# Performance work log

Hardware: AMD Instinct MI355X
Metric: run time of the kernel (lower is better)

Reference implementation:

```python
import jax, jax.numpy as jnp
import numpy as np
from jax import lax

B, T, U, L, V = 256, 256, 512, 256, 64


def lstm_layer(x_seq, Wx, Wh, b):
    """Keras LSTMCell math, gate order i,f,g,o. x_seq: [B,T,D] -> [B,T,U], (h,c)."""
    batch = x_seq.shape[0]
    units = Wh.shape[0]
    h0 = jnp.zeros((batch, units), x_seq.dtype)
    c0 = jnp.zeros((batch, units), x_seq.dtype)

    def step(carry, xt):
        h, c = carry
        z = xt @ Wx + h @ Wh + b  # [B,4U]
        i, f, g, o = jnp.split(z, 4, axis=-1)
        i = jax.nn.sigmoid(i)
        f = jax.nn.sigmoid(f)
        g = jnp.tanh(g)
        o = jax.nn.sigmoid(o)
        c = f * c + i * g
        h = o * jnp.tanh(c)
        return (h, c), h

    xs = jnp.swapaxes(x_seq, 0, 1)  # [T,B,D]
    (h, c), ys = lax.scan(step, (h0, c0), xs)
    return jnp.swapaxes(ys, 0, 1), (h, c)


def run_stack(x, Wx0, Wh0, b0, Wx12, Wh12, b12):
    y, (h, c) = lstm_layer(x, Wx0, Wh0, b0)
    for l in range(2):
        y, (h, c) = lstm_layer(y, Wx12[l], Wh12[l], b12[l])
    return y, h


def setup_inputs() -> dict:
    key = jax.random.key(0)
    ks = jax.random.split(key, 24)

    def u(k, shape, s=0.1):
        return jax.random.uniform(k, shape, jnp.float32, -s, s)

    inp = {}
    inp["tokens"] = jax.random.randint(ks[0], (B, T), 0, V, dtype=jnp.int32)
    inp["eps"] = jax.random.normal(ks[1], (B, L), dtype=jnp.float32)
    inp["emb"] = u(ks[2], (L, V))  # embedding table [latent, vocab] as in source
    # encoder LSTM stack (layer0 input dim V; layers 1,2 input dim U)
    inp["enc_Wx0"] = u(ks[3], (V, 4 * U))
    inp["enc_Wh0"] = u(ks[4], (U, 4 * U))
    inp["enc_b0"] = jnp.zeros((4 * U,), jnp.float32)
    inp["enc_Wx12"] = u(ks[5], (2, U, 4 * U))
    inp["enc_Wh12"] = u(ks[6], (2, U, 4 * U))
    inp["enc_b12"] = jnp.zeros((2, 4 * U), jnp.float32)
    # encoder latent heads
    inp["w_mean"] = u(ks[7], (U, L))
    inp["b_mean"] = jnp.zeros((L,), jnp.float32)
    inp["w_sigma"] = u(ks[8], (U, L))
    inp["b_sigma"] = jnp.zeros((L,), jnp.float32)
    # decoder LSTM stack (layer0 input dim L+V)
    inp["dec_Wx0"] = u(ks[9], (L + V, 4 * U))
    inp["dec_Wh0"] = u(ks[10], (U, 4 * U))
    inp["dec_b0"] = jnp.zeros((4 * U,), jnp.float32)
    inp["dec_Wx12"] = u(ks[11], (2, U, 4 * U))
    inp["dec_Wh12"] = u(ks[12], (2, U, 4 * U))
    inp["dec_b12"] = jnp.zeros((2, 4 * U), jnp.float32)
    # decoder output projection
    inp["dec_W"] = u(ks[13], (U, V))
    inp["dec_b"] = jnp.zeros((V,), jnp.float32)
    return inp


def reference(tokens, eps, emb, enc_Wx0, enc_Wh0, enc_b0, enc_Wx12, enc_Wh12,
              enc_b12, w_mean, b_mean, w_sigma, b_sigma, dec_Wx0, dec_Wh0,
              dec_b0, dec_Wx12, dec_Wh12, dec_b12, dec_W, dec_b):
    # embedding lookup: table [L, V] indexed by token ids -> x: [B, T, V]
    x = emb[tokens]
    # encoder: 3-layer LSTM, take final h of last layer
    _, h = run_stack(x, enc_Wx0, enc_Wh0, enc_b0, enc_Wx12, enc_Wh12, enc_b12)
    mean = h @ w_mean + b_mean
    sigma = h @ w_sigma + b_sigma
    latent = mean + jnp.exp(sigma / 2.0) * eps  # reparameterization
    # tile latent over time and concat with embedded inputs
    z = jnp.broadcast_to(latent[:, None, :], (B, T, L))
    dec_in = jnp.concatenate([z, x], axis=-1)  # [B, T, L+V]
    y, _ = run_stack(dec_in, dec_Wx0, dec_Wh0, dec_b0, dec_Wx12, dec_Wh12, dec_b12)
    logits = y @ dec_W + dec_b  # [B, T, V]
    pred = jnp.argmax(logits, axis=2)  # argmax(softmax) == argmax(logits)
    return (pred, logits)
```

## Files before the change

kernel.cpp:

```cpp
#include <hip/hip_runtime.h>
#include <math.h>

#define B 256
#define T 256
#define U 512
#define L 256
#define V 64
#define G4U 2048
#define BU (B * U)
#define HBUF 262144

typedef __attribute__((ext_vector_type(8))) short bf16x8;
typedef __attribute__((ext_vector_type(16))) float f32x16;

__device__ __forceinline__ unsigned short bf16_hi(float x) {
    union { float f; unsigned int u; } c; c.f = x;
    unsigned int r = c.u + 0x7fffu + ((c.u >> 16) & 1u);
    return (unsigned short)(r >> 16);
}
__device__ __forceinline__ float bf16_f(unsigned short h) {
    union { unsigned int u; float f; } c; c.u = ((unsigned int)h) << 16;
    return c.f;
}

__device__ __forceinline__ void st_coh32(void* p, unsigned int v) {
    asm volatile("global_store_dword %0, %1, off sc0 sc1"
                 :: "v"(p), "v"(v) : "memory");
}
__device__ __forceinline__ unsigned int ld_coh32_wait(const void* p) {
    unsigned int r;
    asm volatile("global_load_dword %0, %1, off sc0 sc1\n\t"
                 "s_waitcnt vmcnt(0)"
                 : "=v"(r) : "v"(p) : "memory");
    return r;
}

__device__ __forceinline__ void flags_wait(int* bar, int wmask, int target, int lane)
{
    if (threadIdx.x < 64) {
        #pragma unroll
        for (int r = 0; r < 4; ++r) {
            if (wmask & (1 << r)) {
                const int fi = (r * 64 + lane) * 16;
                while ((int)ld_coh32_wait(&bar[fi]) < target)
                    __builtin_amdgcn_s_sleep(1);
            }
        }
        __builtin_amdgcn_fence(__ATOMIC_ACQUIRE, "agent");
    }
    __syncthreads();
}
__device__ __forceinline__ void flags_pub(int* bar, int bid, int val)
{
    asm volatile("s_waitcnt vmcnt(0)" ::: "memory");
    __syncthreads();
    if (threadIdx.x == 0)
        st_coh32(&bar[bid * 16], (unsigned int)val);
}

__device__ __forceinline__ void gemm4(const unsigned short* __restrict__ abase,
                                      const unsigned short* bhiB,
                                      const unsigned short* bloB,
                                      int kh8, f32x16& acc)
{
    bf16x8 ah[4], al[4];
    #pragma unroll
    for (int i = 0; i < 4; ++i) {
        ah[i] = *(const bf16x8*)(abase + i * 32 + kh8);
        al[i] = *(const bf16x8*)(abase + i * 32 + 16 + kh8);
    }
    #pragma unroll
    for (int i = 0; i < 4; ++i) {
        bf16x8 bh = *(const bf16x8*)(bhiB + i * 512);
        bf16x8 bl = *(const bf16x8*)(bloB + i * 512);
        acc = __builtin_amdgcn_mfma_f32_32x32x16_bf16(ah[i], bh, acc, 0, 0, 0);
        acc = __builtin_amdgcn_mfma_f32_32x32x16_bf16(ah[i], bl, acc, 0, 0, 0);
        acc = __builtin_amdgcn_mfma_f32_32x32x16_bf16(al[i], bh, acc, 0, 0, 0);
    }
}

template<int NCH>
__device__ __forceinline__ void gemm_sub(const unsigned short* __restrict__ abase,
                                         const unsigned short* bhiB,
                                         const unsigned short* bloB,
                                         f32x16& acc)
{
    constexpr int NB = NCH / 8;
    bf16x8 ah[2][8], al[2][8];
    #pragma unroll
    for (int i = 0; i < 8; ++i) {
        ah[0][i] = *(const bf16x8*)(abase + i * 1024);
        al[0][i] = *(const bf16x8*)(abase + i * 1024 + 512);
    }
    #pragma unroll
    for (int b = 0; b < NB; ++b) {
        const int cur = b & 1, nxt = cur ^ 1;
        if (b + 1 < NB) {
            #pragma unroll
            for (int i = 0; i < 8; ++i) {
                const int c = (b + 1) * 8 + i;
                ah[nxt][i] = *(const bf16x8*)(abase + c * 1024);
                al[nxt][i] = *(const bf16x8*)(abase + c * 1024 + 512);
            }
        }
        #pragma unroll
        for (int i = 0; i < 8; ++i) {
            const int c = b * 8 + i;
            bf16x8 bh = *(const bf16x8*)(bhiB + c * 512);
            bf16x8 bl = *(const bf16x8*)(bloB + c * 512);
            acc = __builtin_amdgcn_mfma_f32_32x32x16_bf16(ah[cur][i], bh, acc, 0, 0, 0);
            acc = __builtin_amdgcn_mfma_f32_32x32x16_bf16(ah[cur][i], bl, acc, 0, 0, 0);
            acc = __builtin_amdgcn_mfma_f32_32x32x16_bf16(al[cur][i], bh, acc, 0, 0, 0);
        }
    }
}

__global__ void __launch_bounds__(512, 1)
vae_stack(const unsigned short* __restrict__ xI,
          const float* __restrict__ Wx0, const float* __restrict__ Wh0,
          const float* __restrict__ Wx1, const float* __restrict__ Wh1,
          const float* __restrict__ Wx2, const float* __restrict__ Wh2,
          const float* __restrict__ cb_base, const float* __restrict__ rb0,
          unsigned short* __restrict__ h,
          const float* __restrict__ projW, const float* __restrict__ projB,
          float* __restrict__ out, int nphase, int* __restrict__ bar)
{
    __shared__ __align__(16) char smem[131072];
    const int nb = gridDim.x;
    const int tid = threadIdx.x;
    const int bid = blockIdx.x;
    const int role = bid >> 6;
    const int ug = bid & 63;
    const int lane = tid & 63;
    const int wv = tid >> 6;
    const int m0 = wv * 32;

    const int allmask = (nb == 256) ? 0b1111 : 0b0111;
    int wmask;
    if      (role == 0) wmask = 0b0011;
    else if (role == 1) wmask = 0b0111;
    else if (role == 2) wmask = (nb == 256) ? 0b1110 : 0b0110;
    else                wmask = 0b0100;

    {
        unsigned int* hz = (unsigned int*)h;
        const int stride = nb * 512;
        for (int i = bid * 512 + tid; i < 786432; i += stride)
            st_coh32(hz + i, 0u);
    }

    auto HP = [&](int layer, int buf) -> unsigned short* {
        return h + (size_t)(layer * 2 + buf) * HBUF;
    };

    if (role < 3) {
        const int K  = (role == 0) ? 576 : 1024;
        const int Dx = (role == 0) ? 64 : 512;
        unsigned short* Whi = (unsigned short*)smem;
        unsigned short* Wlo = (unsigned short*)(smem + 65536);

        const float* WxL = (role == 0) ? Wx0 : ((role == 1) ? Wx1 : Wx2);
        const float* WhL = (role == 0) ? Wh0 : ((role == 1) ? Wh1 : Wh2);
        for (int idx = tid; idx < K * 32; idx += 512) {
            int k = idx >> 5, n = idx & 31, u = n >> 2, g = n & 3;
            int col = g * 512 + ug * 8 + u;
            float w = (k < Dx) ? WxL[(size_t)k * G4U + col]
                               : WhL[(size_t)(k - Dx) * G4U + col];
            unsigned short hi = bf16_hi(w);
            int off = ((k >> 3) * 32 + n) * 8 + (k & 7);
            Whi[off] = hi;
            Wlo[off] = bf16_hi(w - bf16_f(hi));
        }

        const bool userb = (role == 0) && (rb0 != nullptr);
        const float colbias = userb ? 0.0f
                            : cb_base[role * 2048 + ug * 32 + (lane & 31)];
        float cst[16];
        #pragma unroll
        for (int i = 0; i < 16; ++i) cst[i] = 0.0f;

        const int arow = m0 + (lane & 31);
        const int kh8  = (lane >> 5) * 8;
        const int frg  = (lane >> 5) * 256 + (lane & 31) * 8;
        const int lf   = (lane & 31) * 16 + (lane >> 5) * 8;
        const size_t mt = (size_t)wv * 32768;

        flags_pub(bar, bid, 1);
        flags_wait(bar, allmask, 1, lane);

        for (int p = 0; p < nphase; ++p) {
            flags_wait(bar, wmask, p + 1, lane);
            const int t = p - role;
            if (t >= 0 && t < T) {
                const int wr = t & 1, rd = wr ^ 1;
                f32x16 acc;
                #pragma unroll
                for (int i = 0; i < 16; ++i) acc[i] = 0.0f;

                if (role == 0) {
                    gemm4(xI + ((size_t)arow * T + t) * 128,
                          Whi + frg, Wlo + frg, kh8, acc);
                    gemm_sub<32>(HP(0, rd) + mt + lf,
                                 Whi + 4 * 512 + frg, Wlo + 4 * 512 + frg, acc);
                } else {
                    gemm_sub<32>(HP(role - 1, wr) + mt + lf,
                                 Whi + frg, Wlo + frg, acc);
                    gemm_sub<32>(HP(role, rd) + mt + lf,
                                 Whi + 32 * 512 + frg, Wlo + 32 * 512 + frg, acc);
                }

                const int n = lane & 31, g = n & 3, u8 = n >> 2, hi5 = lane >> 5;
                unsigned short* hw = HP(role, wr);
                const int gu = ug * 8 + u8;
                const int cg = gu >> 4, eg = gu & 15;
                const bool g1 = (g & 1), g2 = (g & 2);
                const bool store_t = (g == 0) && !(u8 & 1);
                #pragma unroll
                for (int r = 0; r < 16; ++r) {
                    int ri = (r & 3) + 8 * (r >> 2) + 4 * hi5;
                    float z = acc[r] + colbias;
                    if (userb) z += rb0[(size_t)(m0 + ri) * G4U + ug * 32 + n];
                    float zb = __shfl_xor(z, 1, 64);
                    float zc = __shfl_xor(z, 2, 64);
                    float zd = __shfl_xor(z, 3, 64);
                    float t01 = g1 ? zb : z,  t23 = g1 ? zd : zc;
                    float u01 = g1 ? z  : zb, u23 = g1 ? zc : zd;
                    float zi = g2 ? t23 : t01;
                    float zf = g2 ? u23 : u01;
                    float zG = g2 ? t01 : t23;
                    float zo = g2 ? u01 : u23;
                    float ig = 1.0f / (1.0f + expf(-zi));
                    float fg = 1.0f / (1.0f + expf(-zf));
                    float gg = tanhf(zG);
                    float og = 1.0f / (1.0f + expf(-zo));
                    cst[r] = fg * cst[r] + ig * gg;
                    float hv = og * tanhf(cst[r]);
                    unsigned short hh2 = bf16_hi(hv);
                    unsigned short hl2 = bf16_hi(hv - bf16_f(hh2));
                    unsigned int hh_p = (unsigned int)__shfl_xor((int)hh2, 4, 64);
                    unsigned int hl_p = (unsigned int)__shfl_xor((int)hl2, 4, 64);
                    if (store_t) {
                        size_t ho = mt + (size_t)cg * 1024 + ri * 16 + eg;
                        st_coh32(hw + ho,       (unsigned int)hh2 | (hh_p << 16));
                        st_coh32(hw + ho + 512, (unsigned int)hl2 | (hl_p << 16));
                    }
                }
            }
            flags_pub(bar, bid, p + 2);
        }
    } else {
        float* hrow  = (float*)smem;
        float* parts = (float*)(smem + 8192);
        const int b0p = ug * 4;
        const float pbv = projW ? projB[lane] : 0.0f;
        const int r = wv & 3, kp = wv >> 2, v = lane;
        flags_pub(bar, bid, 1);
        flags_wait(bar, allmask, 1, lane);
        for (int p = 0; p < nphase; ++p) {
            flags_wait(bar, wmask, p + 1, lane);
            const int tp = p - 3;
            if (projW && tp >= 0 && tp < T) {
                {
                    int rr = tid >> 7, kq = (tid & 127) * 4;
                    int grow = b0p + rr;
                    int c = kq >> 4, e = kq & 15;
                    const unsigned short* hb2 = HP(2, tp & 1)
                        + (size_t)(grow >> 5) * 32768 + (size_t)c * 1024
                        + (grow & 31) * 16 + e;
                    ushort4 vh = *(const ushort4*)hb2;
                    ushort4 vl = *(const ushort4*)(hb2 + 512);
                    float4 f;
                    f.x = bf16_f(vh.x) + bf16_f(vl.x);
                    f.y = bf16_f(vh.y) + bf16_f(vl.y);
                    f.z = bf16_f(vh.z) + bf16_f(vl.z);
                    f.w = bf16_f(vh.w) + bf16_f(vl.w);
                    *(float4*)(hrow + rr * 512 + kq) = f;
                }
                __syncthreads();
                float acc = 0.0f;
                const float* wp = projW + (size_t)v * 512 + kp * 256;
                const float* hp = hrow + r * 512 + kp * 256;
                #pragma unroll 8
                for (int q = 0; q < 64; ++q) {
                    float4 w  = *(const float4*)(wp + q * 4);
                    float4 hq = *(const float4*)(hp + q * 4);
                    acc = fmaf(w.x, hq.x, acc); acc = fmaf(w.y, hq.y, acc);
                    acc = fmaf(w.z, hq.z, acc); acc = fmaf(w.w, hq.w, acc);
                }
                if (kp == 1) parts[r * 64 + v] = acc;
                __syncthreads();
                if (kp == 0) {
                    float logit = acc + parts[r * 64 + v] + pbv;
                    int grow = b0p + r;
                    __builtin_nontemporal_store(
                        logit, &out[(size_t)B * T + ((size_t)grow * T + tp) * V + v]);
                    float best = logit; int bi = v;
                    #pragma unroll
                    for (int off = 32; off; off >>= 1) {
                        float ov = __shfl_xor(best, off, 64);
                        int oi  = __shfl_xor(bi, off, 64);
                        if (ov > best || (ov == best && oi < bi)) { best = ov; bi = oi; }
                    }
                    if (v == 0)
                        __builtin_nontemporal_store((float)bi,
                                                    &out[(size_t)grow * T + tp]);
                }
            }
            flags_pub(bar, bid, p + 2);
        }
    }
}

__global__ void embed_split_k(const int* __restrict__ tok, const float* __restrict__ emb,
                              unsigned short* __restrict__ xI)
{
    int idx = blockIdx.x * 256 + threadIdx.x;
    int pos = idx >> 4, q = idx & 15;
    int c = q >> 2, kk4 = (q & 3) * 4;
    int tk = tok[pos];
    float4 v = *(const float4*)(emb + (size_t)tk * V + q * 4);
    ushort4 hh, ll;
    hh.x = bf16_hi(v.x); ll.x = bf16_hi(v.x - bf16_f(hh.x));
    hh.y = bf16_hi(v.y); ll.y = bf16_hi(v.y - bf16_f(hh.y));
    hh.z = bf16_hi(v.z); ll.z = bf16_hi(v.z - bf16_f(hh.z));
    hh.w = bf16_hi(v.w); ll.w = bf16_hi(v.w - bf16_f(hh.w));
    size_t base = (size_t)pos * 128 + c * 32 + kk4;
    *(ushort4*)(xI + base) = hh;
    *(ushort4*)(xI + base + 16) = ll;
}

__global__ void latent_k(const unsigned short* __restrict__ h2,
                         const float* __restrict__ eps,
                         const float* __restrict__ wm, const float* __restrict__ bm,
                         const float* __restrict__ wsig, const float* __restrict__ bs,
                         float* __restrict__ lat)
{
    __shared__ float hr[U];
    int b = blockIdx.x, l = threadIdx.x;
    {
        size_t o1 = (size_t)(b >> 5) * 32768 + (size_t)(l >> 4) * 1024
                  + (b & 31) * 16 + (l & 15);
        int l2 = l + 256;
        size_t o2 = (size_t)(b >> 5) * 32768 + (size_t)(l2 >> 4) * 1024
                  + (b & 31) * 16 + (l2 & 15);
        hr[l]  = bf16_f(h2[o1]) + bf16_f(h2[o1 + 512]);
        hr[l2] = bf16_f(h2[o2]) + bf16_f(h2[o2 + 512]);
    }
    __syncthreads();
    float am = bm[l], as = bs[l];
    for (int k = 0; k < U; ++k) {
        float h = hr[k];
        am = fmaf(h, wm[(size_t)k * L + l], am);
        as = fmaf(h, wsig[(size_t)k * L + l], as);
    }
    lat[(size_t)b * L + l] = am + expf(as * 0.5f) * eps[(size_t)b * L + l];
}

__global__ void xcr_k(const float* __restrict__ lat, const float* __restrict__ Wx0,
                      const float* __restrict__ b0v, float* __restrict__ xcr)
{
    __shared__ float lr[L];
    int b = blockIdx.x >> 3;
    int oc = (blockIdx.x & 7) * 256 + threadIdx.x;
    lr[threadIdx.x] = lat[(size_t)b * L + threadIdx.x];
    __syncthreads();
    float acc = b0v[oc];
    for (int k = 0; k < L; ++k) acc = fmaf(lr[k], Wx0[(size_t)k * G4U + oc], acc);
    int g = oc >> 9, rest = oc & 511, ugi = rest >> 3, u = rest & 7;
    xcr[(size_t)b * G4U + ugi * 32 + u * 4 + g] = acc;
}

__global__ void biasref_k(const float* s0, const float* s1, const float* s2,
                          const float* s3, const float* s4, float* __restrict__ ebr)
{
    int idx = blockIdx.x * 256 + threadIdx.x;
    int which = idx >> 11, oc = idx & 2047;
    const float* s = which == 0 ? s0 : which == 1 ? s1 : which == 2 ? s2
                   : which == 3 ? s3 : s4;
    int g = oc >> 9, rest = oc & 511, ugi = rest >> 3, u = rest & 7;
    ebr[which * 2048 + ugi * 32 + u * 4 + g] = s[oc];
}

__global__ void wtprep_k(const float* __restrict__ W, float* __restrict__ Wt)
{
    int idx = blockIdx.x * 256 + threadIdx.x;
    int k = idx >> 6, v = idx & 63;
    Wt[(size_t)v * 512 + k] = W[idx];
}

__global__ void barinit_k(int* __restrict__ bar)
{
    bar[blockIdx.x * 256 + threadIdx.x] = 0;
}

__global__ void sentinel_k(float* __restrict__ out, float val) { out[threadIdx.x] = val; }

extern "C" void kernel_launch(void* const* d_in, const int* in_sizes, int n_in,
                              void* d_out, int out_size, void* d_ws, size_t ws_size,
                              hipStream_t stream)
{
    const int*   tokens   = (const int*)  d_in[0];
    const float* eps      = (const float*)d_in[1];
    const float* emb      = (const float*)d_in[2];
    const float* enc_Wx0  = (const float*)d_in[3];
    const float* enc_Wh0  = (const float*)d_in[4];
    const float* enc_b0   = (const float*)d_in[5];
    const float* enc_Wx12 = (const float*)d_in[6];
    const float* enc_Wh12 = (const float*)d_in[7];
    const float* enc_b12  = (const float*)d_in[8];
    const float* w_mean   = (const float*)d_in[9];
    const float* b_mean   = (const float*)d_in[10];
    const float* w_sigma  = (const float*)d_in[11];
    const float* b_sigma  = (const float*)d_in[12];
    const float* dec_Wx0  = (const float*)d_in[13];
    const float* dec_Wh0  = (const float*)d_in[14];
    const float* dec_b0   = (const float*)d_in[15];
    const float* dec_Wx12 = (const float*)d_in[16];
    const float* dec_Wh12 = (const float*)d_in[17];
    const float* dec_b12  = (const float*)d_in[18];
    const float* dec_W    = (const float*)d_in[19];
    const float* dec_b    = (const float*)d_in[20];
    float* out = (float*)d_out;

    unsigned short* xI  = (unsigned short*)d_ws;
    unsigned short* h   = xI + (size_t)B * T * 128;
    float* lat = (float*)(h + 6 * (size_t)HBUF);
    float* xcr = lat + (size_t)B * L;
    float* ebr = xcr + (size_t)B * G4U;
    float* Wt  = ebr + 5 * G4U;
    int*   bar = (int*)(Wt + 64 * 512);
    size_t need = (size_t)((char*)(bar + 4096) - (char*)d_ws);
    if (ws_size < need) {
        sentinel_k<<<dim3(1), dim3(64), 0, stream>>>(out, -1.0e6f);
        return;
    }

    const size_t UG = (size_t)U * G4U;

    embed_split_k<<<dim3(B * T * 16 / 256), dim3(256), 0, stream>>>(tokens, emb, xI);
    biasref_k<<<dim3(40), dim3(256), 0, stream>>>(enc_b0, enc_b12, enc_b12 + G4U,
                                                  dec_b12, dec_b12 + G4U, ebr);
    wtprep_k<<<dim3(128), dim3(256), 0, stream>>>(dec_W, Wt);

    auto coop = [&](int grid, const float* Wx0_, const float* Wh0_,
                    const float* Wx1_, const float* Wh1_,
                    const float* Wx2_, const float* Wh2_,
                    const float* cbb, const float* rb,
                    const float* pW, const float* pB, int np) -> hipError_t {
        const unsigned short* a_xI = xI;
        unsigned short* a_h = h;
        float* a_out = out;
        int* a_bar = bar;
        void* args[] = { (void*)&a_xI,
                         (void*)&Wx0_, (void*)&Wh0_, (void*)&Wx1_, (void*)&Wh1_,
                         (void*)&Wx2_, (void*)&Wh2_,
                         (void*)&cbb, (void*)&rb, (void*)&a_h,
                         (void*)&pW, (void*)&pB, (void*)&a_out, (void*)&np,
                         (void*)&a_bar };
        return hipLaunchCooperativeKernel((void*)vae_stack, dim3(grid), dim3(512),
                                          args, 0, stream);
    };

    barinit_k<<<dim3(16), dim3(256), 0, stream>>>(bar);
    hipError_t e1 = coop(192, enc_Wx0, enc_Wh0, enc_Wx12, enc_Wh12,
                         enc_Wx12 + UG, enc_Wh12 + UG,
                         ebr, nullptr, nullptr, nullptr, T + 2);

    latent_k<<<dim3(B), dim3(256), 0, stream>>>(h + 5 * (size_t)HBUF,
                                                eps, w_mean, b_mean, w_sigma, b_sigma, lat);
    xcr_k<<<dim3(2048), dim3(256), 0, stream>>>(lat, dec_Wx0, dec_b0, xcr);

    barinit_k<<<dim3(16), dim3(256), 0, stream>>>(bar);
    hipError_t e2 = coop(256, dec_Wx0 + (size_t)L * G4U, dec_Wh0, dec_Wx12, dec_Wh12,
                         dec_Wx12 + UG, dec_Wh12 + UG,
                         ebr + 2 * G4U, xcr, Wt, dec_b, T + 3);

    if (e1 != hipSuccess || e2 != hipSuccess) {
        sentinel_k<<<dim3(1), dim3(64), 0, stream>>>(out, -3.0e6f);
    }
}
```

Baseline: 14.04 ms.

## Use 64-slot hidden-state ring buffers to relax inter-layer wavefront sync

Replaces the double-buffered per-layer hidden state with a 64-slot ring per layer. Each role now waits only on its upstream producer every phase and on its downstream consumer only once it is 56 phases ahead, so layers are no longer held in tight lockstep. The per-phase agent acquire fence is dropped in favour of one fence every 32 phases, relying on coherent sc0/sc1 loads and stores. This costs much more workspace and a larger hidden-state footprint in cache, and the sparser fence risks stale reads if coherence is not guaranteed.

```diff
diff --git a/kernel.cpp b/kernel.cpp
--- a/kernel.cpp
+++ b/kernel.cpp
@@ -7,8 +7,8 @@
 #define L 256
 #define V 64
 #define G4U 2048
-#define BU (B * U)
 #define HBUF 262144
+#define SLOTS 64
 
 typedef __attribute__((ext_vector_type(8))) short bf16x8;
 typedef __attribute__((ext_vector_type(16))) float f32x16;
@@ -46,7 +46,6 @@
                     __builtin_amdgcn_s_sleep(1);
             }
         }
-        __builtin_amdgcn_fence(__ATOMIC_ACQUIRE, "agent");
     }
     __syncthreads();
 }
@@ -56,6 +55,15 @@
     __syncthreads();
     if (threadIdx.x == 0)
         st_coh32(&bar[bid * 16], (unsigned int)val);
+}
+
+__device__ __forceinline__ void ring_fence(int p)
+{
+    if ((p & 31) == 0) {
+        if (threadIdx.x == 0)
+            __builtin_amdgcn_fence(__ATOMIC_ACQUIRE, "agent");
+        __syncthreads();
+    }
 }
 
 __device__ __forceinline__ void gemm4(const unsigned short* __restrict__ abase,
@@ -127,6 +135,7 @@
 {
     __shared__ __align__(16) char smem[131072];
     const int nb = gridDim.x;
+    const bool hasProj = (nb == 256);
     const int tid = threadIdx.x;
     const int bid = blockIdx.x;
     const int role = bid >> 6;
@@ -134,23 +143,19 @@
     const int lane = tid & 63;
     const int wv = tid >> 6;
     const int m0 = wv * 32;
-
-    const int allmask = (nb == 256) ? 0b1111 : 0b0111;
-    int wmask;
-    if      (role == 0) wmask = 0b0011;
-    else if (role == 1) wmask = 0b0111;
-    else if (role == 2) wmask = (nb == 256) ? 0b1110 : 0b0110;
-    else                wmask = 0b0100;
+    const int allmask = hasProj ? 0b1111 : 0b0111;
 
     {
         unsigned int* hz = (unsigned int*)h;
         const int stride = nb * 512;
-        for (int i = bid * 512 + tid; i < 786432; i += stride)
-            st_coh32(hz + i, 0u);
-    }
-
-    auto HP = [&](int layer, int buf) -> unsigned short* {
-        return h + (size_t)(layer * 2 + buf) * HBUF;
+        for (int i = bid * 512 + tid; i < 393216; i += stride) {
+            int l = i >> 17, off = i & 131071;
+            st_coh32(hz + ((size_t)(l * SLOTS + 63) * 131072 + off), 0u);
+        }
+    }
+
+    auto HP = [&](int layer, int t) -> unsigned short* {
+        return h + ((size_t)(layer * SLOTS) + (t & (SLOTS - 1))) * HBUF;
     };
 
     if (role < 3) {
@@ -189,10 +194,19 @@
         flags_wait(bar, allmask, 1, lane);
 
         for (int p = 0; p < nphase; ++p) {
-            flags_wait(bar, wmask, p + 1, lane);
+            if (role == 0) {
+                flags_wait(bar, 0b0001, p + 1, lane);
+                if (p >= 56) flags_wait(bar, 0b0010, p - 55, lane);
+            } else if (role == 1) {
+                flags_wait(bar, 0b0011, p + 1, lane);
+                if (p >= 56) flags_wait(bar, 0b0100, p - 55, lane);
+            } else {
+                flags_wait(bar, 0b0110, p + 1, lane);
+                if (hasProj && p >= 56) flags_wait(bar, 0b1000, p - 55, lane);
+            }
+            ring_fence(p);
             const int t = p - role;
             if (t >= 0 && t < T) {
-                const int wr = t & 1, rd = wr ^ 1;
                 f32x16 acc;
                 #pragma unroll
                 for (int i = 0; i < 16; ++i) acc[i] = 0.0f;
@@ -200,17 +214,17 @@
                 if (role == 0) {
                     gemm4(xI + ((size_t)arow * T + t) * 128,
                           Whi + frg, Wlo + frg, kh8, acc);
-                    gemm_sub<32>(HP(0, rd) + mt + lf,
+                    gemm_sub<32>(HP(0, t - 1) + mt + lf,
                                  Whi + 4 * 512 + frg, Wlo + 4 * 512 + frg, acc);
                 } else {
-                    gemm_sub<32>(HP(role - 1, wr) + mt + lf,
+                    gemm_sub<32>(HP(role - 1, t) + mt + lf,
                                  Whi + frg, Wlo + frg, acc);
-                    gemm_sub<32>(HP(role, rd) + mt + lf,
+                    gemm_sub<32>(HP(role, t - 1) + mt + lf,
                                  Whi + 32 * 512 + frg, Wlo + 32 * 512 + frg, acc);
                 }
 
                 const int n = lane & 31, g = n & 3, u8 = n >> 2, hi5 = lane >> 5;
-                unsigned short* hw = HP(role, wr);
+                unsigned short* hw = HP(role, t);
                 const int gu = ug * 8 + u8;
                 const int cg = gu >> 4, eg = gu & 15;
                 const bool g1 = (g & 1), g2 = (g & 2);
@@ -257,14 +271,15 @@
         flags_pub(bar, bid, 1);
         flags_wait(bar, allmask, 1, lane);
         for (int p = 0; p < nphase; ++p) {
-            flags_wait(bar, wmask, p + 1, lane);
+            flags_wait(bar, 0b0100, p + 1, lane);
+            ring_fence(p);
             const int tp = p - 3;
             if (projW && tp >= 0 && tp < T) {
                 {
                     int rr = tid >> 7, kq = (tid & 127) * 4;
                     int grow = b0p + rr;
                     int c = kq >> 4, e = kq & 15;
-                    const unsigned short* hb2 = HP(2, tp & 1)
+                    const unsigned short* hb2 = HP(2, tp)
                         + (size_t)(grow >> 5) * 32768 + (size_t)c * 1024
                         + (grow & 31) * 16 + e;
                     ushort4 vh = *(const ushort4*)hb2;
@@ -424,7 +439,7 @@
 
     unsigned short* xI  = (unsigned short*)d_ws;
     unsigned short* h   = xI + (size_t)B * T * 128;
-    float* lat = (float*)(h + 6 * (size_t)HBUF);
+    float* lat = (float*)(h + (size_t)3 * SLOTS * HBUF);
     float* xcr = lat + (size_t)B * L;
     float* ebr = xcr + (size_t)B * G4U;
     float* Wt  = ebr + 5 * G4U;
@@ -466,7 +481,7 @@
                          enc_Wx12 + UG, enc_Wh12 + UG,
                          ebr, nullptr, nullptr, nullptr, T + 2);
 
-    latent_k<<<dim3(B), dim3(256), 0, stream>>>(h + 5 * (size_t)HBUF,
+    latent_k<<<dim3(B), dim3(256), 0, stream>>>(h + (size_t)(2 * SLOTS + 63) * HBUF,
                                                 eps, w_mean, b_mean, w_sigma, b_sigma, lat);
     xcr_k<<<dim3(2048), dim3(256), 0, stream>>>(lat, dec_Wx0, dec_b0, xcr);
 
```

Result: faster. 13.02 ms (-7.2%).
